# Optimization experiments

Measured on AMD Instinct MI355X. Metric: run time of the kernel, lower is better.

The kernel has to match this reference:

```python
import jax, jax.numpy as jnp
import numpy as np

B, S, D, H = 4, 2048, 512, 8
HD = D // H  # head_dim = 64


def setup_inputs() -> dict:
    key = jax.random.key(0)
    ks = jax.random.split(key, 11)
    sc = 1.0 / np.sqrt(D)
    inp = {
        "query": jax.random.normal(ks[0], (B, S, D), jnp.float32),
        "key": jax.random.normal(ks[1], (B, S, D), jnp.float32),
        "value": jax.random.normal(ks[2], (B, S, D), jnp.float32),
        "Wq": jax.random.normal(ks[3], (D, D), jnp.float32) * sc,
        "bq": jax.random.normal(ks[4], (D,), jnp.float32) * sc,
        "Wk": jax.random.normal(ks[5], (D, D), jnp.float32) * sc,
        "bk": jax.random.normal(ks[6], (D,), jnp.float32) * sc,
        "Wv": jax.random.normal(ks[7], (D, D), jnp.float32) * sc,
        "bv": jax.random.normal(ks[8], (D,), jnp.float32) * sc,
        "Wo": jax.random.normal(ks[9], (D, D), jnp.float32) * sc,
        "bo": jax.random.normal(ks[10], (D,), jnp.float32) * sc,
    }
    return inp


def reference(query, key, value, Wq, bq, Wk, bk, Wv, bv, Wo, bo):
    batch = query.shape[0]
    # Linear projections (x @ W + b)
    q = query @ Wq + bq
    k = key @ Wk + bk
    v = value @ Wv + bv
    # NOTE: original uses .view(B*H, -1, head_dim) — a raw row-major reshape
    # (interleaves seq and head dims). Replicated exactly with jnp.reshape.
    q = q.reshape(batch * H, -1, HD)
    k = k.reshape(batch * H, -1, HD)
    v = v.reshape(batch * H, -1, HD)
    # scores: [B*H, L, L], fully materialized as in the original bmm path
    scores = jnp.einsum("bqd,bkd->bqk", q, k) / jnp.sqrt(jnp.float32(HD))
    probs = jax.nn.softmax(scores, axis=-1)  # dropout=0.0 -> identity
    out = jnp.einsum("bqk,bkd->bqd", probs, v)
    out = out.reshape(batch, -1, D)
    out = out @ Wo + bo
    return out, probs
```

## Files before the change

### kernel.cpp

```cpp
#include <hip/hip_runtime.h>


typedef __attribute__((ext_vector_type(4))) float fvec4;
typedef __attribute__((ext_vector_type(4))) float f32x4;
typedef __attribute__((ext_vector_type(8))) short bf16x8;
typedef __attribute__((ext_vector_type(4))) short bf16x4;

__device__ inline unsigned short f2bf_rne(float x) {
    unsigned u = __builtin_bit_cast(unsigned, x);
    unsigned r = (u + 0x7FFFu + ((u >> 16) & 1u)) >> 16;
    return (unsigned short)r;
}
__device__ inline float bf2f(unsigned short h) {
    unsigned u = ((unsigned)h) << 16;
    return __builtin_bit_cast(float, u);
}

template <bool SPLIT>
__global__ __launch_bounds__(256) void gemm_bt(
    const float* __restrict__ A, int lda, long long sA,
    const float* __restrict__ B, int ldb, long long sB,
    float* __restrict__ C, int ldc, long long sC,
    const float* __restrict__ bias, float scale, int K)
{
    __shared__ __align__(16) unsigned short Ah[64][40];
    __shared__ __align__(16) unsigned short Al[64][40];
    __shared__ __align__(16) unsigned short Bh[64][40];
    __shared__ __align__(16) unsigned short Bl[64][40];

    const int tid  = threadIdx.x;
    const int lane = tid & 63;
    const int wv   = tid >> 6;
    const int z    = blockIdx.z;
    A += (long long)z * sA;
    B += (long long)z * sB;
    C += (long long)z * sC;
    const int row0 = blockIdx.x * 64;
    const int col0 = blockIdx.y * 64;

    f32x4 acc[4];
#pragma unroll
    for (int i = 0; i < 4; i++)
#pragma unroll
        for (int r = 0; r < 4; r++) acc[i][r] = 0.f;

    const int lr = tid >> 2;
    const int lc = (tid & 3) * 8;
    const int ar = (wv << 4) + (lane & 15);
    const int kk = (lane >> 4) << 3;

    for (int k0 = 0; k0 < K; k0 += 32) {
        const float* ap = A + (long long)(row0 + lr) * lda + k0 + lc;
        fvec4 a0 = *(const fvec4*)ap;
        fvec4 a1 = *(const fvec4*)(ap + 4);
        const float* bp = B + (long long)(col0 + lr) * ldb + k0 + lc;
        fvec4 b0 = *(const fvec4*)bp;
        fvec4 b1 = *(const fvec4*)(bp + 4);

        __syncthreads();
#pragma unroll
        for (int j = 0; j < 4; j++) {
            unsigned short h;
            h = f2bf_rne(a0[j]); Ah[lr][lc + j] = h;
            if (SPLIT) Al[lr][lc + j] = f2bf_rne(a0[j] - bf2f(h));
            h = f2bf_rne(a1[j]); Ah[lr][lc + 4 + j] = h;
            if (SPLIT) Al[lr][lc + 4 + j] = f2bf_rne(a1[j] - bf2f(h));
            h = f2bf_rne(b0[j]); Bh[lr][lc + j] = h;
            if (SPLIT) Bl[lr][lc + j] = f2bf_rne(b0[j] - bf2f(h));
            h = f2bf_rne(b1[j]); Bh[lr][lc + 4 + j] = h;
            if (SPLIT) Bl[lr][lc + 4 + j] = f2bf_rne(b1[j] - bf2f(h));
        }
        __syncthreads();

        bf16x8 aH = *(const bf16x8*)&Ah[ar][kk];
        bf16x8 aL;
        if (SPLIT) aL = *(const bf16x8*)&Al[ar][kk];
#pragma unroll
        for (int cb = 0; cb < 4; cb++) {
            const int br = (cb << 4) + (lane & 15);
            bf16x8 bH = *(const bf16x8*)&Bh[br][kk];
            acc[cb] = __builtin_amdgcn_mfma_f32_16x16x32_bf16(aH, bH, acc[cb], 0, 0, 0);
            if (SPLIT) {
                bf16x8 bL = *(const bf16x8*)&Bl[br][kk];
                acc[cb] = __builtin_amdgcn_mfma_f32_16x16x32_bf16(aH, bL, acc[cb], 0, 0, 0);
                acc[cb] = __builtin_amdgcn_mfma_f32_16x16x32_bf16(aL, bH, acc[cb], 0, 0, 0);
            }
        }
    }

#pragma unroll
    for (int cb = 0; cb < 4; cb++) {
#pragma unroll
        for (int r = 0; r < 4; r++) {
            const int row = row0 + (wv << 4) + ((lane >> 4) << 2) + r;
            const int col = col0 + (cb << 4) + (lane & 15);
            float v = acc[cb][r] * scale;
            if (bias) v += bias[col];
            C[(long long)row * ldc + col] = v;
        }
    }
}

__global__ __launch_bounds__(256) void proj_qkv(
    const float* __restrict__ X0, const float* __restrict__ X1, const float* __restrict__ X2,
    const float* __restrict__ WT,
    const float* __restrict__ b0_, const float* __restrict__ b1_, const float* __restrict__ b2_,
    unsigned short* __restrict__ qh, unsigned short* __restrict__ ql,
    unsigned short* __restrict__ kh, unsigned short* __restrict__ kl,
    unsigned short* __restrict__ vh)
{
    __shared__ __align__(16) unsigned short Ah[64][40];
    __shared__ __align__(16) unsigned short Al[64][40];
    __shared__ __align__(16) unsigned short Bh[64][40];
    __shared__ __align__(16) unsigned short Bl[64][40];

    const int tid  = threadIdx.x;
    const int lane = tid & 63;
    const int wv   = tid >> 6;
    const int z    = blockIdx.z;
    const float* A    = z == 0 ? X0 : z == 1 ? X1 : X2;
    const float* B    = WT + (long long)z * 262144;
    const float* bias = z == 0 ? b0_ : z == 1 ? b1_ : b2_;
    unsigned short* Oh = z == 0 ? qh : z == 1 ? kh : vh;
    unsigned short* Ol = z == 0 ? ql : z == 1 ? kl : nullptr;

    const int row0 = blockIdx.x * 64;
    const int col0 = blockIdx.y * 64;

    f32x4 acc[4];
#pragma unroll
    for (int i = 0; i < 4; i++)
#pragma unroll
        for (int r = 0; r < 4; r++) acc[i][r] = 0.f;

    const int lr = tid >> 2;
    const int lc = (tid & 3) * 8;
    const int ar = (wv << 4) + (lane & 15);
    const int kk = (lane >> 4) << 3;

    for (int k0 = 0; k0 < 512; k0 += 32) {
        const float* ap = A + (long long)(row0 + lr) * 512 + k0 + lc;
        fvec4 a0 = *(const fvec4*)ap;
        fvec4 a1 = *(const fvec4*)(ap + 4);
        const float* bp = B + (long long)(col0 + lr) * 512 + k0 + lc;
        fvec4 b0 = *(const fvec4*)bp;
        fvec4 b1 = *(const fvec4*)(bp + 4);

        __syncthreads();
#pragma unroll
        for (int j = 0; j < 4; j++) {
            unsigned short h;
            h = f2bf_rne(a0[j]); Ah[lr][lc + j] = h;     Al[lr][lc + j] = f2bf_rne(a0[j] - bf2f(h));
            h = f2bf_rne(a1[j]); Ah[lr][lc + 4 + j] = h; Al[lr][lc + 4 + j] = f2bf_rne(a1[j] - bf2f(h));
            h = f2bf_rne(b0[j]); Bh[lr][lc + j] = h;     Bl[lr][lc + j] = f2bf_rne(b0[j] - bf2f(h));
            h = f2bf_rne(b1[j]); Bh[lr][lc + 4 + j] = h; Bl[lr][lc + 4 + j] = f2bf_rne(b1[j] - bf2f(h));
        }
        __syncthreads();

        bf16x8 aH = *(const bf16x8*)&Ah[ar][kk];
        bf16x8 aL = *(const bf16x8*)&Al[ar][kk];
#pragma unroll
        for (int cb = 0; cb < 4; cb++) {
            const int br = (cb << 4) + (lane & 15);
            bf16x8 bH = *(const bf16x8*)&Bh[br][kk];
            bf16x8 bL = *(const bf16x8*)&Bl[br][kk];
            acc[cb] = __builtin_amdgcn_mfma_f32_16x16x32_bf16(aH, bH, acc[cb], 0, 0, 0);
            acc[cb] = __builtin_amdgcn_mfma_f32_16x16x32_bf16(aH, bL, acc[cb], 0, 0, 0);
            acc[cb] = __builtin_amdgcn_mfma_f32_16x16x32_bf16(aL, bH, acc[cb], 0, 0, 0);
        }
    }

#pragma unroll
    for (int cb = 0; cb < 4; cb++) {
#pragma unroll
        for (int r = 0; r < 4; r++) {
            const int row = row0 + (wv << 4) + ((lane >> 4) << 2) + r;
            const int col = col0 + (cb << 4) + (lane & 15);
            float v = acc[cb][r] + bias[col];
            unsigned short h = f2bf_rne(v);
            Oh[(long long)row * 512 + col] = h;
            if (Ol) Ol[(long long)row * 512 + col] = f2bf_rne(v - bf2f(h));
        }
    }
}

__global__ __launch_bounds__(256) void transpose512(
    const float* __restrict__ W0, const float* __restrict__ W1,
    const float* __restrict__ W2, const float* __restrict__ W3,
    float* __restrict__ out)
{
    const float* W = blockIdx.z == 0 ? W0 : blockIdx.z == 1 ? W1 : blockIdx.z == 2 ? W2 : W3;
    float* o = out + (long long)blockIdx.z * 262144;
    __shared__ float t[32][33];
    const int x = threadIdx.x, y = threadIdx.y;
    const int n0 = blockIdx.x * 32, k0 = blockIdx.y * 32;
#pragma unroll
    for (int j = 0; j < 4; j++) t[y + 8 * j][x] = W[(long long)(k0 + y + 8 * j) * 512 + n0 + x];
    __syncthreads();
#pragma unroll
    for (int j = 0; j < 4; j++) o[(long long)(n0 + y + 8 * j) * 512 + k0 + x] = t[x][y + 8 * j];
}

__global__ __launch_bounds__(256) void vtrans2(
    const unsigned short* __restrict__ vh, unsigned short* __restrict__ vt)
{
    __shared__ __align__(16) unsigned short t[64][80];
    const int tid = threadIdx.x;
    const int c = blockIdx.y;
    const int l0 = blockIdx.x * 64;
    const long long cb = (long long)c * 131072;
    const int rrow = tid >> 3, ccol = (tid & 7) * 8;
#pragma unroll
    for (int rr = 0; rr < 2; rr++)
        *(bf16x8*)&t[rrow + rr * 32][ccol] =
            *(const bf16x8*)(vh + cb + (long long)(l0 + rrow + rr * 32) * 64 + ccol);
    __syncthreads();
#pragma unroll
    for (int rr = 0; rr < 2; rr++) {
        const int hd = rrow + rr * 32;
        bf16x8 o;
#pragma unroll
        for (int q2 = 0; q2 < 8; q2++) o[q2] = (short)t[ccol + q2][hd];
        *(bf16x8*)(vt + cb + (long long)hd * 2048 + l0 + ccol) = o;
    }
}

__global__ __launch_bounds__(256) void fused_attn(
    const unsigned short* __restrict__ qh, const unsigned short* __restrict__ ql,
    const unsigned short* __restrict__ kh, const unsigned short* __restrict__ kl,
    const unsigned short* __restrict__ vt,
    float* __restrict__ probs, float* __restrict__ ao)
{
    __shared__ __align__(16) unsigned short skh[64][80];
    __shared__ __align__(16) unsigned short skl[64][80];
    __shared__ __align__(16) unsigned short svt[64][80];
    __shared__ __align__(16) unsigned short sP[4][16][68];

    const int tid  = threadIdx.x;
    const int lane = tid & 63;
    const int wv   = tid >> 6;
    const int c    = blockIdx.y;
    const int row0 = blockIdx.x * 64;
    const long long cbase = (long long)c * 131072;

    const int l15 = lane & 15;
    const int kk  = (lane >> 4) << 3;

    const int arow = row0 + wv * 16 + l15;
    bf16x8 aH[2], aL[2];
    {
        const unsigned short* qp  = qh + cbase + (long long)arow * 64;
        const unsigned short* qlp = ql + cbase + (long long)arow * 64;
        aH[0] = *(const bf16x8*)(qp + kk);
        aH[1] = *(const bf16x8*)(qp + 32 + kk);
        aL[0] = *(const bf16x8*)(qlp + kk);
        aL[1] = *(const bf16x8*)(qlp + 32 + kk);
    }

    const int srow = tid >> 3;
    const int scol = (tid & 7) * 8;

    f32x4 acc_o[4];
#pragma unroll
    for (int i = 0; i < 4; i++)
#pragma unroll
        for (int r = 0; r < 4; r++) acc_o[i][r] = 0.f;
    float rsum[4] = {0.f, 0.f, 0.f, 0.f};

    for (int j = 0; j < 32; j++) {
        __syncthreads();
        const long long ktb = cbase + (long long)j * 4096;
        const long long vtb = cbase + j * 64;
#pragma unroll
        for (int rr = 0; rr < 2; rr++) {
            const int r2 = srow + rr * 32;
            *(bf16x8*)&skh[r2][scol] = *(const bf16x8*)(kh + ktb + (long long)r2 * 64 + scol);
            *(bf16x8*)&skl[r2][scol] = *(const bf16x8*)(kl + ktb + (long long)r2 * 64 + scol);
            *(bf16x8*)&svt[r2][scol] = *(const bf16x8*)(vt + vtb + (long long)r2 * 2048 + scol);
        }
        __syncthreads();

        f32x4 s[4];
#pragma unroll
        for (int cb = 0; cb < 4; cb++)
#pragma unroll
            for (int r = 0; r < 4; r++) s[cb][r] = 0.f;
#pragma unroll
        for (int ks = 0; ks < 2; ks++) {
#pragma unroll
            for (int cb = 0; cb < 4; cb++) {
                const int col = cb * 16 + l15;
                bf16x8 bH = *(const bf16x8*)&skh[col][ks * 32 + kk];
                bf16x8 bL = *(const bf16x8*)&skl[col][ks * 32 + kk];
                s[cb] = __builtin_amdgcn_mfma_f32_16x16x32_bf16(aH[ks], bH, s[cb], 0, 0, 0);
                s[cb] = __builtin_amdgcn_mfma_f32_16x16x32_bf16(aH[ks], bL, s[cb], 0, 0, 0);
                s[cb] = __builtin_amdgcn_mfma_f32_16x16x32_bf16(aL[ks], bH, s[cb], 0, 0, 0);
            }
        }
#pragma unroll
        for (int cb = 0; cb < 4; cb++) {
#pragma unroll
            for (int r = 0; r < 4; r++) {
                float p = __expf(s[cb][r] * 0.125f);
                rsum[r] += p;
                sP[wv][(lane >> 4) * 4 + r][cb * 16 + l15] = f2bf_rne(p);
            }
        }
#pragma unroll
        for (int ks = 0; ks < 2; ks++) {
            bf16x4 p0 = *(const bf16x4*)&sP[wv][l15][ks * 32 + kk];
            bf16x4 p1 = *(const bf16x4*)&sP[wv][l15][ks * 32 + kk + 4];
            bf16x8 pa;
#pragma unroll
            for (int q2 = 0; q2 < 4; q2++) { pa[q2] = p0[q2]; pa[4 + q2] = p1[q2]; }
#pragma unroll
            for (int co = 0; co < 4; co++) {
                bf16x8 bV = *(const bf16x8*)&svt[co * 16 + l15][ks * 32 + kk];
                acc_o[co] = __builtin_amdgcn_mfma_f32_16x16x32_bf16(pa, bV, acc_o[co], 0, 0, 0);
            }
        }
    }

#pragma unroll
    for (int r = 0; r < 4; r++) {
        float s = rsum[r];
        s += __shfl_xor(s, 1, 64);
        s += __shfl_xor(s, 2, 64);
        s += __shfl_xor(s, 4, 64);
        s += __shfl_xor(s, 8, 64);
        rsum[r] = 1.f / s;
    }

#pragma unroll
    for (int co = 0; co < 4; co++) {
#pragma unroll
        for (int r = 0; r < 4; r++) {
            const int orow = row0 + wv * 16 + (lane >> 4) * 4 + r;
            ao[cbase + (long long)orow * 64 + co * 16 + l15] = acc_o[co][r] * rsum[r];
        }
    }

    for (int j = 0; j < 32; j++) {
        __syncthreads();
        const long long ktb = cbase + (long long)j * 4096;
#pragma unroll
        for (int rr = 0; rr < 2; rr++) {
            const int r2 = srow + rr * 32;
            *(bf16x8*)&skh[r2][scol] = *(const bf16x8*)(kh + ktb + (long long)r2 * 64 + scol);
            *(bf16x8*)&skl[r2][scol] = *(const bf16x8*)(kl + ktb + (long long)r2 * 64 + scol);
        }
        __syncthreads();

        f32x4 s[4];
#pragma unroll
        for (int cb = 0; cb < 4; cb++)
#pragma unroll
            for (int r = 0; r < 4; r++) s[cb][r] = 0.f;
#pragma unroll
        for (int ks = 0; ks < 2; ks++) {
#pragma unroll
            for (int cb = 0; cb < 4; cb++) {
                const int col = cb * 16 + l15;
                bf16x8 bH = *(const bf16x8*)&skh[col][ks * 32 + kk];
                bf16x8 bL = *(const bf16x8*)&skl[col][ks * 32 + kk];
                s[cb] = __builtin_amdgcn_mfma_f32_16x16x32_bf16(aH[ks], bH, s[cb], 0, 0, 0);
                s[cb] = __builtin_amdgcn_mfma_f32_16x16x32_bf16(aH[ks], bL, s[cb], 0, 0, 0);
                s[cb] = __builtin_amdgcn_mfma_f32_16x16x32_bf16(aL[ks], bH, s[cb], 0, 0, 0);
            }
        }
        float* pb = probs + (long long)c * 4194304 +
                    (long long)(row0 + wv * 16 + (lane >> 4) * 4) * 2048 + j * 64;
#pragma unroll
        for (int cb = 0; cb < 4; cb++) {
#pragma unroll
            for (int r = 0; r < 4; r++) {
                pb[(long long)r * 2048 + cb * 16 + l15] = __expf(s[cb][r] * 0.125f) * rsum[r];
            }
        }
    }
}

extern "C" void kernel_launch(void* const* d_in, const int* in_sizes, int n_in,
                              void* d_out, int out_size, void* d_ws, size_t ws_size,
                              hipStream_t stream)
{
    const float* query = (const float*)d_in[0];
    const float* key_  = (const float*)d_in[1];
    const float* value = (const float*)d_in[2];
    const float* Wq = (const float*)d_in[3];
    const float* bq = (const float*)d_in[4];
    const float* Wk = (const float*)d_in[5];
    const float* bk = (const float*)d_in[6];
    const float* Wv = (const float*)d_in[7];
    const float* bv = (const float*)d_in[8];
    const float* Wo = (const float*)d_in[9];
    const float* bo = (const float*)d_in[10];

    float* out   = (float*)d_out;
    float* probs = out + 4194304LL;

    char* w = (char*)d_ws;
    unsigned short* qh = (unsigned short*)(w);
    unsigned short* ql = (unsigned short*)(w + (8LL << 20));
    unsigned short* kh = (unsigned short*)(w + (16LL << 20));
    unsigned short* kl = (unsigned short*)(w + (24LL << 20));
    unsigned short* vh = (unsigned short*)(w + (32LL << 20));
    unsigned short* vt = (unsigned short*)(w + (40LL << 20));
    float*          WT = (float*)(w + (48LL << 20));
    float*          ao = (float*)(w + (52LL << 20));

    transpose512<<<dim3(16, 16, 4), dim3(32, 8, 1), 0, stream>>>(Wq, Wk, Wv, Wo, WT);

    proj_qkv<<<dim3(128, 8, 3), 256, 0, stream>>>(query, key_, value, WT, bq, bk, bv,
                                                  qh, ql, kh, kl, vh);

    vtrans2<<<dim3(32, 32, 1), 256, 0, stream>>>(vh, vt);

    fused_attn<<<dim3(32, 32, 1), 256, 0, stream>>>(qh, ql, kh, kl, vt, probs, ao);

    gemm_bt<true><<<dim3(128, 8, 1), 256, 0, stream>>>(ao, 512, 0, WT + 786432, 512, 0,
                                                       out, 512, 0, bo, 1.f, 512);
}
```

Before: 357.7 us.

## Pre-split inputs to bf16 hi/lo, prefetch tiles in registers, remap attention blocks

Adds separate kernels that split the fp32 inputs and transposed weights into bf16 hi/lo pairs once. The probs output buffer is reused as scratch for the split inputs. Both projection GEMMs and the attention kernel now load the next tile into registers while computing the current one, a software prefetch. The attention kernel also remaps block IDs to change locality and writes its output already split for the output projection. This removes per-tile conversion work from the GEMM inner loops and hides global load latency, at the cost of extra passes over memory and more live registers.

```diff
diff --git a/kernel.cpp b/kernel.cpp
--- a/kernel.cpp
+++ b/kernel.cpp
@@ -16,27 +16,69 @@
     return __builtin_bit_cast(float, u);
 }
 
-template <bool SPLIT>
-__global__ __launch_bounds__(256) void gemm_bt(
-    const float* __restrict__ A, int lda, long long sA,
-    const float* __restrict__ B, int ldb, long long sB,
-    float* __restrict__ C, int ldc, long long sC,
-    const float* __restrict__ bias, float scale, int K)
+__global__ __launch_bounds__(256) void split3(
+    const float* __restrict__ X0, const float* __restrict__ X1, const float* __restrict__ X2,
+    unsigned short* __restrict__ Hb, unsigned short* __restrict__ Lb)
+{
+    const float* X = blockIdx.z == 0 ? X0 : blockIdx.z == 1 ? X1 : X2;
+    unsigned short* H = Hb + (long long)blockIdx.z * 4194304;
+    unsigned short* L = Lb + (long long)blockIdx.z * 4194304;
+    const long long i = (long long)(blockIdx.x * 256 + threadIdx.x) * 8;
+    fvec4 a = *(const fvec4*)(X + i);
+    fvec4 b = *(const fvec4*)(X + i + 4);
+    bf16x8 h, l;
+#pragma unroll
+    for (int j = 0; j < 4; j++) {
+        unsigned short hh = f2bf_rne(a[j]);
+        h[j] = (short)hh; l[j] = (short)f2bf_rne(a[j] - bf2f(hh));
+        hh = f2bf_rne(b[j]);
+        h[4 + j] = (short)hh; l[4 + j] = (short)f2bf_rne(b[j] - bf2f(hh));
+    }
+    *(bf16x8*)(H + i) = h;
+    *(bf16x8*)(L + i) = l;
+}
+
+__global__ __launch_bounds__(256) void wtrans_split(
+    const float* __restrict__ W0, const float* __restrict__ W1,
+    const float* __restrict__ W2, const float* __restrict__ W3,
+    unsigned short* __restrict__ TH, unsigned short* __restrict__ TL)
+{
+    const float* W = blockIdx.z == 0 ? W0 : blockIdx.z == 1 ? W1 : blockIdx.z == 2 ? W2 : W3;
+    unsigned short* th = TH + (long long)blockIdx.z * 262144;
+    unsigned short* tl = TL + (long long)blockIdx.z * 262144;
+    __shared__ float t[32][33];
+    const int x = threadIdx.x, y = threadIdx.y;
+    const int n0 = blockIdx.x * 32, k0 = blockIdx.y * 32;
+#pragma unroll
+    for (int j = 0; j < 4; j++) t[y + 8 * j][x] = W[(long long)(k0 + y + 8 * j) * 512 + n0 + x];
+    __syncthreads();
+#pragma unroll
+    for (int j = 0; j < 4; j++) {
+        float v = t[x][y + 8 * j];
+        unsigned short h = f2bf_rne(v);
+        th[(long long)(n0 + y + 8 * j) * 512 + k0 + x] = h;
+        tl[(long long)(n0 + y + 8 * j) * 512 + k0 + x] = f2bf_rne(v - bf2f(h));
+    }
+}
+
+template <bool SPLIT_OUT>
+__global__ __launch_bounds__(256) void gemm_bs(
+    const unsigned short* __restrict__ AH, const unsigned short* __restrict__ AL, long long sAz,
+    const unsigned short* __restrict__ BH, const unsigned short* __restrict__ BL, long long sBz,
+    const float* __restrict__ b0, const float* __restrict__ b1, const float* __restrict__ b2,
+    unsigned short* __restrict__ OH, unsigned short* __restrict__ OL,
+    float* __restrict__ OF, long long sOz)
 {
     __shared__ __align__(16) unsigned short Ah[64][40];
     __shared__ __align__(16) unsigned short Al[64][40];
     __shared__ __align__(16) unsigned short Bh[64][40];
     __shared__ __align__(16) unsigned short Bl[64][40];
 
-    const int tid  = threadIdx.x;
-    const int lane = tid & 63;
-    const int wv   = tid >> 6;
-    const int z    = blockIdx.z;
-    A += (long long)z * sA;
-    B += (long long)z * sB;
-    C += (long long)z * sC;
-    const int row0 = blockIdx.x * 64;
-    const int col0 = blockIdx.y * 64;
+    const int tid = threadIdx.x, lane = tid & 63, wv = tid >> 6;
+    const int z = blockIdx.z;
+    AH += z * sAz; AL += z * sAz; BH += z * sBz; BL += z * sBz;
+    const float* bias = z == 0 ? b0 : z == 1 ? b1 : b2;
+    const int row0 = blockIdx.x * 64, col0 = blockIdx.y * 64;
 
     f32x4 acc[4];
 #pragma unroll
@@ -49,112 +91,22 @@
     const int ar = (wv << 4) + (lane & 15);
     const int kk = (lane >> 4) << 3;
 
-    for (int k0 = 0; k0 < K; k0 += 32) {
-        const float* ap = A + (long long)(row0 + lr) * lda + k0 + lc;
-        fvec4 a0 = *(const fvec4*)ap;
-        fvec4 a1 = *(const fvec4*)(ap + 4);
-        const float* bp = B + (long long)(col0 + lr) * ldb + k0 + lc;
-        fvec4 b0 = *(const fvec4*)bp;
-        fvec4 b1 = *(const fvec4*)(bp + 4);
-
-        __syncthreads();
-#pragma unroll
-        for (int j = 0; j < 4; j++) {
-            unsigned short h;
-            h = f2bf_rne(a0[j]); Ah[lr][lc + j] = h;
-            if (SPLIT) Al[lr][lc + j] = f2bf_rne(a0[j] - bf2f(h));
-            h = f2bf_rne(a1[j]); Ah[lr][lc + 4 + j] = h;
-            if (SPLIT) Al[lr][lc + 4 + j] = f2bf_rne(a1[j] - bf2f(h));
-            h = f2bf_rne(b0[j]); Bh[lr][lc + j] = h;
-            if (SPLIT) Bl[lr][lc + j] = f2bf_rne(b0[j] - bf2f(h));
-            h = f2bf_rne(b1[j]); Bh[lr][lc + 4 + j] = h;
-            if (SPLIT) Bl[lr][lc + 4 + j] = f2bf_rne(b1[j] - bf2f(h));
-        }
-        __syncthreads();
-
-        bf16x8 aH = *(const bf16x8*)&Ah[ar][kk];
-        bf16x8 aL;
-        if (SPLIT) aL = *(const bf16x8*)&Al[ar][kk];
-#pragma unroll
-        for (int cb = 0; cb < 4; cb++) {
-            const int br = (cb << 4) + (lane & 15);
-            bf16x8 bH = *(const bf16x8*)&Bh[br][kk];
-            acc[cb] = __builtin_amdgcn_mfma_f32_16x16x32_bf16(aH, bH, acc[cb], 0, 0, 0);
-            if (SPLIT) {
-                bf16x8 bL = *(const bf16x8*)&Bl[br][kk];
-                acc[cb] = __builtin_amdgcn_mfma_f32_16x16x32_bf16(aH, bL, acc[cb], 0, 0, 0);
-                acc[cb] = __builtin_amdgcn_mfma_f32_16x16x32_bf16(aL, bH, acc[cb], 0, 0, 0);
-            }
-        }
-    }
-
-#pragma unroll
-    for (int cb = 0; cb < 4; cb++) {
-#pragma unroll
-        for (int r = 0; r < 4; r++) {
-            const int row = row0 + (wv << 4) + ((lane >> 4) << 2) + r;
-            const int col = col0 + (cb << 4) + (lane & 15);
-            float v = acc[cb][r] * scale;
-            if (bias) v += bias[col];
-            C[(long long)row * ldc + col] = v;
-        }
-    }
-}
-
-__global__ __launch_bounds__(256) void proj_qkv(
-    const float* __restrict__ X0, const float* __restrict__ X1, const float* __restrict__ X2,
-    const float* __restrict__ WT,
-    const float* __restrict__ b0_, const float* __restrict__ b1_, const float* __restrict__ b2_,
-    unsigned short* __restrict__ qh, unsigned short* __restrict__ ql,
-    unsigned short* __restrict__ kh, unsigned short* __restrict__ kl,
-    unsigned short* __restrict__ vh)
-{
-    __shared__ __align__(16) unsigned short Ah[64][40];
-    __shared__ __align__(16) unsigned short Al[64][40];
-    __shared__ __align__(16) unsigned short Bh[64][40];
-    __shared__ __align__(16) unsigned short Bl[64][40];
-
-    const int tid  = threadIdx.x;
-    const int lane = tid & 63;
-    const int wv   = tid >> 6;
-    const int z    = blockIdx.z;
-    const float* A    = z == 0 ? X0 : z == 1 ? X1 : X2;
-    const float* B    = WT + (long long)z * 262144;
-    const float* bias = z == 0 ? b0_ : z == 1 ? b1_ : b2_;
-    unsigned short* Oh = z == 0 ? qh : z == 1 ? kh : vh;
-    unsigned short* Ol = z == 0 ? ql : z == 1 ? kl : nullptr;
-
-    const int row0 = blockIdx.x * 64;
-    const int col0 = blockIdx.y * 64;
-
-    f32x4 acc[4];
-#pragma unroll
-    for (int i = 0; i < 4; i++)
-#pragma unroll
-        for (int r = 0; r < 4; r++) acc[i][r] = 0.f;
-
-    const int lr = tid >> 2;
-    const int lc = (tid & 3) * 8;
-    const int ar = (wv << 4) + (lane & 15);
-    const int kk = (lane >> 4) << 3;
-
-    for (int k0 = 0; k0 < 512; k0 += 32) {
-        const float* ap = A + (long long)(row0 + lr) * 512 + k0 + lc;
-        fvec4 a0 = *(const fvec4*)ap;
-        fvec4 a1 = *(const fvec4*)(ap + 4);
-        const float* bp = B + (long long)(col0 + lr) * 512 + k0 + lc;
-        fvec4 b0 = *(const fvec4*)bp;
-        fvec4 b1 = *(const fvec4*)(bp + 4);
-
-        __syncthreads();
-#pragma unroll
-        for (int j = 0; j < 4; j++) {
-            unsigned short h;
-            h = f2bf_rne(a0[j]); Ah[lr][lc + j] = h;     Al[lr][lc + j] = f2bf_rne(a0[j] - bf2f(h));
-            h = f2bf_rne(a1[j]); Ah[lr][lc + 4 + j] = h; Al[lr][lc + 4 + j] = f2bf_rne(a1[j] - bf2f(h));
-            h = f2bf_rne(b0[j]); Bh[lr][lc + j] = h;     Bl[lr][lc + j] = f2bf_rne(b0[j] - bf2f(h));
-            h = f2bf_rne(b1[j]); Bh[lr][lc + 4 + j] = h; Bl[lr][lc + 4 + j] = f2bf_rne(b1[j] - bf2f(h));
-        }
+    bf16x8 ra_h, ra_l, rb_h, rb_l;
+    auto ldregs = [&](int k0) {
+        ra_h = *(const bf16x8*)(AH + (long long)(row0 + lr) * 512 + k0 + lc);
+        ra_l = *(const bf16x8*)(AL + (long long)(row0 + lr) * 512 + k0 + lc);
+        rb_h = *(const bf16x8*)(BH + (long long)(col0 + lr) * 512 + k0 + lc);
+        rb_l = *(const bf16x8*)(BL + (long long)(col0 + lr) * 512 + k0 + lc);
+    };
+
+    ldregs(0);
+    for (int t = 0; t < 16; t++) {
+        __syncthreads();
+        *(bf16x8*)&Ah[lr][lc] = ra_h;
+        *(bf16x8*)&Al[lr][lc] = ra_l;
+        *(bf16x8*)&Bh[lr][lc] = rb_h;
+        *(bf16x8*)&Bl[lr][lc] = rb_l;
+        if (t < 15) ldregs((t + 1) * 32);
         __syncthreads();
 
         bf16x8 aH = *(const bf16x8*)&Ah[ar][kk];
@@ -174,31 +126,19 @@
     for (int cb = 0; cb < 4; cb++) {
 #pragma unroll
         for (int r = 0; r < 4; r++) {
-            const int row = row0 + (wv << 4) + ((lane >> 4) << 2) + r;
+            const long long row = row0 + (wv << 4) + ((lane >> 4) << 2) + r;
             const int col = col0 + (cb << 4) + (lane & 15);
-            float v = acc[cb][r] + bias[col];
-            unsigned short h = f2bf_rne(v);
-            Oh[(long long)row * 512 + col] = h;
-            if (Ol) Ol[(long long)row * 512 + col] = f2bf_rne(v - bf2f(h));
-        }
-    }
-}
-
-__global__ __launch_bounds__(256) void transpose512(
-    const float* __restrict__ W0, const float* __restrict__ W1,
-    const float* __restrict__ W2, const float* __restrict__ W3,
-    float* __restrict__ out)
-{
-    const float* W = blockIdx.z == 0 ? W0 : blockIdx.z == 1 ? W1 : blockIdx.z == 2 ? W2 : W3;
-    float* o = out + (long long)blockIdx.z * 262144;
-    __shared__ float t[32][33];
-    const int x = threadIdx.x, y = threadIdx.y;
-    const int n0 = blockIdx.x * 32, k0 = blockIdx.y * 32;
-#pragma unroll
-    for (int j = 0; j < 4; j++) t[y + 8 * j][x] = W[(long long)(k0 + y + 8 * j) * 512 + n0 + x];
-    __syncthreads();
-#pragma unroll
-    for (int j = 0; j < 4; j++) o[(long long)(n0 + y + 8 * j) * 512 + k0 + x] = t[x][y + 8 * j];
+            float val = acc[cb][r] + bias[col];
+            if constexpr (SPLIT_OUT) {
+                unsigned short h = f2bf_rne(val);
+                (OH + z * sOz)[row * 512 + col] = h;
+                if (z != 2)
+                    (OL + z * sOz)[row * 512 + col] = f2bf_rne(val - bf2f(h));
+            } else {
+                (OF + z * sOz)[row * 512 + col] = val;
+            }
+        }
+    }
 }
 
 __global__ __launch_bounds__(256) void vtrans2(
@@ -229,36 +169,74 @@
     const unsigned short* __restrict__ qh, const unsigned short* __restrict__ ql,
     const unsigned short* __restrict__ kh, const unsigned short* __restrict__ kl,
     const unsigned short* __restrict__ vt,
-    float* __restrict__ probs, float* __restrict__ ao)
+    float* __restrict__ probs,
+    unsigned short* __restrict__ aoh, unsigned short* __restrict__ aol)
 {
     __shared__ __align__(16) unsigned short skh[64][80];
     __shared__ __align__(16) unsigned short skl[64][80];
     __shared__ __align__(16) unsigned short svt[64][80];
     __shared__ __align__(16) unsigned short sP[4][16][68];
 
-    const int tid  = threadIdx.x;
-    const int lane = tid & 63;
-    const int wv   = tid >> 6;
-    const int c    = blockIdx.y;
-    const int row0 = blockIdx.x * 64;
+    const int tid = threadIdx.x, lane = tid & 63, wv = tid >> 6;
+
+    const int orig = blockIdx.y * 32 + blockIdx.x;
+    const int myid = (orig & 7) * 128 + (orig >> 3);
+    const int c    = myid >> 5;
+    const int row0 = (myid & 31) * 64;
     const long long cbase = (long long)c * 131072;
 
-    const int l15 = lane & 15;
-    const int kk  = (lane >> 4) << 3;
+    const int l15 = lane & 15, g = lane >> 4, kk = g * 8;
+    const int srow = tid >> 3;
+    const int scol = (tid & 7) * 8;
+    const int p_r0 = g * 4;
 
     const int arow = row0 + wv * 16 + l15;
     bf16x8 aH[2], aL[2];
     {
         const unsigned short* qp  = qh + cbase + (long long)arow * 64;
         const unsigned short* qlp = ql + cbase + (long long)arow * 64;
-        aH[0] = *(const bf16x8*)(qp + kk);
-        aH[1] = *(const bf16x8*)(qp + 32 + kk);
-        aL[0] = *(const bf16x8*)(qlp + kk);
-        aL[1] = *(const bf16x8*)(qlp + 32 + kk);
-    }
-
-    const int srow = tid >> 3;
-    const int scol = (tid & 7) * 8;
+        aH[0] = *(const bf16x8*)(qp + kk);   aH[1] = *(const bf16x8*)(qp + 32 + kk);
+        aL[0] = *(const bf16x8*)(qlp + kk);  aL[1] = *(const bf16x8*)(qlp + 32 + kk);
+    }
+
+    bf16x8 rkh[2], rkl[2], rvt[2];
+    auto ld1 = [&](int j) {
+        const long long ktb = cbase + (long long)j * 4096;
+        const long long vtb = cbase + j * 64;
+#pragma unroll
+        for (int rr = 0; rr < 2; rr++) {
+            const int r2 = srow + rr * 32;
+            rkh[rr] = *(const bf16x8*)(kh + ktb + (long long)r2 * 64 + scol);
+            rkl[rr] = *(const bf16x8*)(kl + ktb + (long long)r2 * 64 + scol);
+            rvt[rr] = *(const bf16x8*)(vt + vtb + (long long)r2 * 2048 + scol);
+        }
+    };
+    auto st1 = [&]() {
+#pragma unroll
+        for (int rr = 0; rr < 2; rr++) {
+            const int r2 = srow + rr * 32;
+            *(bf16x8*)&skh[r2][scol] = rkh[rr];
+            *(bf16x8*)&skl[r2][scol] = rkl[rr];
+            *(bf16x8*)&svt[r2][scol] = rvt[rr];
+        }
+    };
+    auto ld2 = [&](int j) {
+        const long long ktb = cbase + (long long)j * 4096;
+#pragma unroll
+        for (int rr = 0; rr < 2; rr++) {
+            const int r2 = srow + rr * 32;
+            rkh[rr] = *(const bf16x8*)(kh + ktb + (long long)r2 * 64 + scol);
+            rkl[rr] = *(const bf16x8*)(kl + ktb + (long long)r2 * 64 + scol);
+        }
+    };
+    auto st2 = [&]() {
+#pragma unroll
+        for (int rr = 0; rr < 2; rr++) {
+            const int r2 = srow + rr * 32;
+            *(bf16x8*)&skh[r2][scol] = rkh[rr];
+            *(bf16x8*)&skl[r2][scol] = rkl[rr];
+        }
+    };
 
     f32x4 acc_o[4];
 #pragma unroll
@@ -267,17 +245,11 @@
         for (int r = 0; r < 4; r++) acc_o[i][r] = 0.f;
     float rsum[4] = {0.f, 0.f, 0.f, 0.f};
 
+    ld1(0);
     for (int j = 0; j < 32; j++) {
         __syncthreads();
-        const long long ktb = cbase + (long long)j * 4096;
-        const long long vtb = cbase + j * 64;
-#pragma unroll
-        for (int rr = 0; rr < 2; rr++) {
-            const int r2 = srow + rr * 32;
-            *(bf16x8*)&skh[r2][scol] = *(const bf16x8*)(kh + ktb + (long long)r2 * 64 + scol);
-            *(bf16x8*)&skl[r2][scol] = *(const bf16x8*)(kl + ktb + (long long)r2 * 64 + scol);
-            *(bf16x8*)&svt[r2][scol] = *(const bf16x8*)(vt + vtb + (long long)r2 * 2048 + scol);
-        }
+        st1();
+        if (j < 31) ld1(j + 1);
         __syncthreads();
 
         f32x4 s[4];
@@ -303,7 +275,7 @@
             for (int r = 0; r < 4; r++) {
                 float p = __expf(s[cb][r] * 0.125f);
                 rsum[r] += p;
-                sP[wv][(lane >> 4) * 4 + r][cb * 16 + l15] = f2bf_rne(p);
+                sP[wv][p_r0 + r][cb * 16 + l15] = f2bf_rne(p);
             }
         }
 #pragma unroll
@@ -335,20 +307,19 @@
     for (int co = 0; co < 4; co++) {
 #pragma unroll
         for (int r = 0; r < 4; r++) {
-            const int orow = row0 + wv * 16 + (lane >> 4) * 4 + r;
-            ao[cbase + (long long)orow * 64 + co * 16 + l15] = acc_o[co][r] * rsum[r];
-        }
-    }
-
+            const long long oi = cbase + (long long)(row0 + wv * 16 + p_r0 + r) * 64 + co * 16 + l15;
+            float o = acc_o[co][r] * rsum[r];
+            unsigned short h = f2bf_rne(o);
+            aoh[oi] = h;
+            aol[oi] = f2bf_rne(o - bf2f(h));
+        }
+    }
+
+    ld2(0);
     for (int j = 0; j < 32; j++) {
         __syncthreads();
-        const long long ktb = cbase + (long long)j * 4096;
-#pragma unroll
-        for (int rr = 0; rr < 2; rr++) {
-            const int r2 = srow + rr * 32;
-            *(bf16x8*)&skh[r2][scol] = *(const bf16x8*)(kh + ktb + (long long)r2 * 64 + scol);
-            *(bf16x8*)&skl[r2][scol] = *(const bf16x8*)(kl + ktb + (long long)r2 * 64 + scol);
-        }
+        st2();
+        if (j < 31) ld2(j + 1);
         __syncthreads();
 
         f32x4 s[4];
@@ -369,7 +340,7 @@
             }
         }
         float* pb = probs + (long long)c * 4194304 +
-                    (long long)(row0 + wv * 16 + (lane >> 4) * 4) * 2048 + j * 64;
+                    (long long)(row0 + wv * 16 + p_r0) * 2048 + j * 64;
 #pragma unroll
         for (int cb = 0; cb < 4; cb++) {
 #pragma unroll
@@ -399,25 +370,32 @@
     float* out   = (float*)d_out;
     float* probs = out + 4194304LL;
 
+    unsigned short* XH = (unsigned short*)probs;
+    unsigned short* XL = XH + 3 * 4194304LL;
+
+    const long long MiB = 1LL << 20;
     char* w = (char*)d_ws;
-    unsigned short* qh = (unsigned short*)(w);
-    unsigned short* ql = (unsigned short*)(w + (8LL << 20));
-    unsigned short* kh = (unsigned short*)(w + (16LL << 20));
-    unsigned short* kl = (unsigned short*)(w + (24LL << 20));
-    unsigned short* vh = (unsigned short*)(w + (32LL << 20));
-    unsigned short* vt = (unsigned short*)(w + (40LL << 20));
-    float*          WT = (float*)(w + (48LL << 20));
-    float*          ao = (float*)(w + (52LL << 20));
-
-    transpose512<<<dim3(16, 16, 4), dim3(32, 8, 1), 0, stream>>>(Wq, Wk, Wv, Wo, WT);
-
-    proj_qkv<<<dim3(128, 8, 3), 256, 0, stream>>>(query, key_, value, WT, bq, bk, bv,
-                                                  qh, ql, kh, kl, vh);
-
-    vtrans2<<<dim3(32, 32, 1), 256, 0, stream>>>(vh, vt);
-
-    fused_attn<<<dim3(32, 32, 1), 256, 0, stream>>>(qh, ql, kh, kl, vt, probs, ao);
-
-    gemm_bt<true><<<dim3(128, 8, 1), 256, 0, stream>>>(ao, 512, 0, WT + 786432, 512, 0,
-                                                       out, 512, 0, bo, 1.f, 512);
-}
+    unsigned short* QKVH = (unsigned short*)(w + 0 * MiB);
+    unsigned short* QKVL = (unsigned short*)(w + 24 * MiB);
+    unsigned short* WTH  = (unsigned short*)(w + 40 * MiB);
+    unsigned short* WTL  = (unsigned short*)(w + 42 * MiB);
+    unsigned short* VT   = (unsigned short*)(w + 44 * MiB);
+    unsigned short* AOH  = (unsigned short*)(w + 52 * MiB);
+    unsigned short* AOL  = (unsigned short*)(w + 60 * MiB);
+
+    split3<<<dim3(2048, 1, 3), 256, 0, stream>>>(query, key_, value, XH, XL);
+    wtrans_split<<<dim3(16, 16, 4), dim3(32, 8, 1), 0, stream>>>(Wq, Wk, Wv, Wo, WTH, WTL);
+
+    gemm_bs<true><<<dim3(128, 8, 3), 256, 0, stream>>>(
+        XH, XL, 4194304, WTH, WTL, 262144, bq, bk, bv,
+        QKVH, QKVL, nullptr, 4194304);
+
+    vtrans2<<<dim3(32, 32, 1), 256, 0, stream>>>(QKVH + 2 * 4194304LL, VT);
+
+    fused_attn<<<dim3(32, 32, 1), 256, 0, stream>>>(
+        QKVH, QKVL, QKVH + 4194304LL, QKVL + 4194304LL, VT, probs, AOH, AOL);
+
+    gemm_bs<false><<<dim3(128, 8, 1), 256, 0, stream>>>(
+        AOH, AOL, 0, WTH + 3 * 262144LL, WTL + 3 * 262144LL, 0, bo, bo, bo,
+        nullptr, nullptr, out, 0);
+}
```

Result: faster. 313.2 us (-12.4%).
